# Optimization experiments

Measured on AMD Instinct MI355X. Metric: run time of the kernel, lower is better.

The kernel has to match this reference:

```python
import jax, jax.numpy as jnp
import numpy as np

E, K, CAP = 6, 2, 192
ALPHA, LOAD_PEN, MIN_USE, TEMP = 0.7, 2.0, 0.05, 1.0
BN_EPS = 1e-5
NEG = -1e30


def conv3x3(x, w, b=None):
    y = jax.lax.conv_general_dilated(x, w, (1, 1), 'SAME',
                                     dimension_numbers=('NCHW', 'OIHW', 'NCHW'))
    if b is not None:
        y = y + b[None, :, None, None]
    return y


def bn_eval(x, g, b):
    # fresh BatchNorm buffers: running_mean=0, running_var=1
    s = g / jnp.sqrt(1.0 + BN_EPS)
    return x * s[None, :, None, None] + b[None, :, None, None]


def maxpool2(x):
    return jax.lax.reduce_window(x, -jnp.inf, jax.lax.max,
                                 (1, 1, 2, 2), (1, 1, 2, 2), 'VALID')


def avgpool_to2(x):
    B, C, H, W = x.shape
    return x.reshape(B, C, 2, H // 2, 2, W // 2).mean(axis=(3, 5))


def expert_forward(p, x):
    h = jax.nn.relu(bn_eval(conv3x3(x, p['c1w'], p['c1b']), p['b1g'], p['b1b']))
    h = maxpool2(h)  # 32 -> 16
    h = jax.nn.relu(bn_eval(conv3x3(h, p['c2w'], p['c2b']), p['b2g'], p['b2b']))
    h = jax.nn.relu(bn_eval(conv3x3(h, p['c3w'], p['c3b']), p['b3g'], p['b3b']))
    h = maxpool2(h)  # 16 -> 8
    h = jax.nn.relu(bn_eval(conv3x3(h, p['c4w'], p['c4b']), p['b4g'], p['b4b']))
    h = jax.nn.relu(bn_eval(conv3x3(h, p['c5w'], p['c5b']), p['b5g'], p['b5b']))
    feat = h.mean(axis=(2, 3))                       # global avg pool -> [B, c3]
    f = jax.nn.relu(feat @ p['fw'].T + p['fb'])      # [B, feat_dim]
    return f @ p['cw'].T + p['cb']                   # [B, num_classes]


def moe_forward(x, t_c1w, t_b1g, t_b1b, t_c2w, t_b2g, t_b2b, t_fcw, t_fcb,
                g1w, g1b, g2w, g2b,
                e_c1w, e_c1b, e_b1g, e_b1b, e_c2w, e_c2b, e_b2g, e_b2b,
                e_c3w, e_c3b, e_b3g, e_b3b, e_c4w, e_c4b, e_b4g, e_b4b,
                e_c5w, e_c5b, e_b5g, e_b5b, e_fw, e_fb, e_cw, e_cb, ema):
    B = x.shape[0]
    # --- routing trunk ---
    h = jax.nn.relu(bn_eval(conv3x3(x, t_c1w), t_b1g, t_b1b))
    h = jax.nn.relu(bn_eval(conv3x3(h, t_c2w), t_b2g, t_b2b))
    h = avgpool_to2(maxpool2(h)).reshape(B, -1)      # [B, 128]
    rf = jax.nn.relu(h @ t_fcw.T + t_fcb)            # [B, routing_dim]
    # --- gate (eval: no dropout, no noise) ---
    g = jax.nn.relu(rf @ g1w.T + g1b)
    gate_scores = (g @ g2w.T + g2b) / TEMP           # [B, E]
    # --- all experts on full batch (dense, as in source) ---
    ep = {'c1w': e_c1w, 'c1b': e_c1b, 'b1g': e_b1g, 'b1b': e_b1b,
          'c2w': e_c2w, 'c2b': e_c2b, 'b2g': e_b2g, 'b2b': e_b2b,
          'c3w': e_c3w, 'c3b': e_c3b, 'b3g': e_b3g, 'b3b': e_b3b,
          'c4w': e_c4w, 'c4b': e_c4b, 'b4g': e_b4g, 'b4b': e_b4b,
          'c5w': e_c5w, 'c5b': e_c5b, 'b5g': e_b5g, 'b5b': e_b5b,
          'fw': e_fw, 'fb': e_fb, 'cw': e_cw, 'cb': e_cb}
    logits_e = jax.vmap(expert_forward, in_axes=(0, None))(ep, x)  # [E, B, C]
    logits_e = jnp.transpose(logits_e, (1, 0, 2))                   # [B, E, C]
    # confidence = -entropy = sum p*log(p)
    logp = jax.nn.log_softmax(logits_e, axis=2)
    conf = (jnp.exp(logp) * jnp.log(jnp.exp(logp) + 1e-12)).sum(axis=2)  # [B, E]
    # --- balanced scores ---
    combined = ALPHA * gate_scores + (1.0 - ALPHA) * conf
    boost = jnp.where(ema < MIN_USE, (MIN_USE - ema) * 10.0, 0.0)
    combined = combined + boost[None, :]
    balanced = combined - LOAD_PEN * ema[None, :]
    # --- greedy capacity-constrained dispatch (deterministic order, eval) ---
    _, topk_idx = jax.lax.top_k(balanced, K)          # [B, K]

    def step(loads, idxs):
        l = loads[idxs]                                # [K]
        fits = l < CAP
        first = jnp.argmax(fits)                       # first expert with room
        fallback = idxs[jnp.argmin(l)]
        chosen = jnp.where(fits.any(), idxs[first], fallback)
        return loads.at[chosen].add(1.0), chosen

    _, chosen = jax.lax.scan(step, jnp.zeros((E,), balanced.dtype), topk_idx)
    D = jax.nn.one_hot(chosen, E, dtype=bool)          # [B, E]
    # --- weighted combine ---
    masked = jnp.where(D, balanced, NEG)
    w = jax.nn.softmax(masked, axis=1) * D.astype(balanced.dtype)
    w = w / (w.sum(axis=1, keepdims=True) + 1e-12)
    logits_final = (w[:, :, None] * logits_e).sum(axis=1)  # [B, C]
    return logits_final, balanced, D


def _params(key):
    ks = iter(jax.random.split(key, 64))
    rd, rd2, fd, nc, c1, c2, c3 = 64, 32, 128, 10, 32, 64, 128

    def w(shape, fan):
        return jax.random.normal(next(ks), shape, jnp.float32) * np.sqrt(2.0 / fan)

    p = {}
    p['t_c1w'] = w((32, 3, 3, 3), 32 * 9); p['t_b1g'] = jnp.ones(32); p['t_b1b'] = jnp.zeros(32)
    p['t_c2w'] = w((32, 32, 3, 3), 32 * 9); p['t_b2g'] = jnp.ones(32); p['t_b2b'] = jnp.zeros(32)
    p['t_fcw'] = w((rd, 128), rd); p['t_fcb'] = jnp.zeros(rd)
    p['g1w'] = w((rd2, rd), rd2); p['g1b'] = jnp.zeros(rd2)
    p['g2w'] = w((E, rd2), E); p['g2b'] = jnp.zeros(E)
    for i, (ci, co) in enumerate([(3, c1), (c1, c2), (c2, c2), (c2, c3), (c3, c3)], 1):
        p[f'e_c{i}w'] = w((E, co, ci, 3, 3), co * 9)
        p[f'e_c{i}b'] = jnp.zeros((E, co))
        p[f'e_b{i}g'] = jnp.ones((E, co))
        p[f'e_b{i}b'] = jnp.zeros((E, co))
    p['e_fw'] = w((E, fd, c3), fd); p['e_fb'] = jnp.zeros((E, fd))
    p['e_cw'] = w((E, nc, fd), nc); p['e_cb'] = jnp.zeros((E, nc))
    p['ema'] = jnp.ones((E,), jnp.float32) / E
    return p


def setup_inputs() -> dict:
    key = jax.random.key(0)
    kx, kp = jax.random.split(key)
    inp = {'x': jax.random.normal(kx, (1024, 3, 32, 32), jnp.float32)}
    inp.update(_params(kp))
    return inp


def reference(x, t_c1w, t_b1g, t_b1b, t_c2w, t_b2g, t_b2b, t_fcw, t_fcb,
              g1w, g1b, g2w, g2b,
              e_c1w, e_c1b, e_b1g, e_b1b, e_c2w, e_c2b, e_b2g, e_b2b,
              e_c3w, e_c3b, e_b3g, e_b3b, e_c4w, e_c4b, e_b4g, e_b4b,
              e_c5w, e_c5b, e_b5g, e_b5b, e_fw, e_fb, e_cw, e_cb, ema):
    return moe_forward(x, t_c1w, t_b1g, t_b1b, t_c2w, t_b2g, t_b2b, t_fcw, t_fcb,
                       g1w, g1b, g2w, g2b,
                       e_c1w, e_c1b, e_b1g, e_b1b, e_c2w, e_c2b, e_b2g, e_b2b,
                       e_c3w, e_c3b, e_b3g, e_b3b, e_c4w, e_c4b, e_b4g, e_b4b,
                       e_c5w, e_c5b, e_b5g, e_b5b, e_fw, e_fb, e_cw, e_cb, ema)
```

## Files before the change

### kernel.cpp

```cpp
#include <hip/hip_runtime.h>
#include <math.h>

#define B_ 1024
#define E_ 6

typedef _Float16 half8 __attribute__((ext_vector_type(8)));
typedef float f32x4 __attribute__((ext_vector_type(4)));

__device__ __forceinline__ unsigned short h_bits(_Float16 h) {
    union { _Float16 f; unsigned short u; } c; c.f = h; return c.u;
}
__device__ __forceinline__ unsigned int splitpack(float v) {
    _Float16 h = (_Float16)v;
    _Float16 l = (_Float16)((v - (float)h) * 2048.0f);
    return (unsigned int)h_bits(h) | ((unsigned int)h_bits(l) << 16);
}
__device__ __forceinline__ int bswz(int fi, int p) { return fi ^ (((p >> 1) & 3) << 3); }

__global__ void prep_w(const float* __restrict__ w, const float* __restrict__ g,
                       float* __restrict__ wout, int CO, int CI, int total) {
    int i = blockIdx.x * 256 + threadIdx.x;
    if (i >= total) return;
    int k = i % 9;
    int t = i / 9;
    int ci = t % CI; t /= CI;
    int co = t % CO;
    int e  = t / CO;
    float s = g[e * CO + co] * (1.0f / sqrtf(1.0f + 1e-5f));
    wout[(((long)(e * CI + ci) * 9 + k) * CO) + co] = w[i] * s;
}

__global__ void prep_b(const float* __restrict__ cb, const float* __restrict__ g,
                       const float* __restrict__ bb, float* __restrict__ bout, int N) {
    int i = blockIdx.x * 256 + threadIdx.x;
    if (i >= N) return;
    float s = g[i] * (1.0f / sqrtf(1.0f + 1e-5f));
    float c = (cb != nullptr) ? cb[i] : 0.0f;
    bout[i] = c * s + bb[i];
}

__global__ void prep_wfrag(const float* __restrict__ w, const float* __restrict__ g,
                           _Float16* __restrict__ out, int CI, int CO, int total) {
    int i = blockIdx.x * 256 + threadIdx.x;
    if (i >= total) return;
    const int NC = CI / 32;
    const int NB = CO / 16;
    int j = i & 7;
    int lane = (i >> 3) & 63;
    int rest = i >> 9;
    int chunk = rest % NC; rest /= NC;
    int tap = rest % 9; rest /= 9;
    int nbg = rest % NB;
    int e = rest / NB;
    int co = nbg * 16 + (lane & 15);
    int ci = chunk * 32 + ((lane >> 4) * 8) + j;
    float s = g[e * CO + co] * (1.0f / sqrtf(1.0f + 1e-5f));
    float v = w[(((long)(e * CO + co) * CI + ci) * 9) + tap] * s;
    _Float16 hi = (_Float16)v;
    _Float16 lo = (_Float16)((v - (float)hi) * 2048.0f);
    long perE = (long)NB * 9 * NC * 2 * 512;
    long F0 = ((long)(nbg * 9 + tap) * NC + chunk) * 2;
    long base = (long)e * perE + F0 * 512 + lane * 8 + j;
    out[base] = hi;
    out[base + 512] = lo;
}

template <int CI, int CO, int H, int TS, int CO_BLK, int CI_CHUNK, bool POOL, int OUTMODE>
__launch_bounds__(256)
__global__ void conv3x3(const float* __restrict__ in, const float* __restrict__ wt,
                        const float* __restrict__ bias, void* __restrict__ outv) {
// ... 209 lines not shown
            for (int nb = 0; nb < 2; ++nb)
#pragma unroll
                for (int mb = 0; mb < 4; ++mb)
                    accL[mb * 2 + nb] = __builtin_amdgcn_mfma_f32_16x16x32_f16(
                        ah[mb], bl[nb], accL[mb * 2 + nb], 0, 0, 0);
#pragma unroll
            for (int nb = 0; nb < 2; ++nb)
#pragma unroll
                for (int mb = 0; mb < 4; ++mb)
                    accL[mb * 2 + nb] = __builtin_amdgcn_mfma_f32_16x16x32_f16(
                        al[mb], bh[nb], accL[mb * 2 + nb], 0, 0, 0);
        }

    const float inv2048 = 1.0f / 2048.0f;
    float bv[2];
#pragma unroll
    for (int nb = 0; nb < 2; ++nb) bv[nb] = bias[nb * 16 + l15];
    float avg[2] = {0.0f, 0.0f};
#pragma unroll
    for (int k = 0; k < 2; ++k)
#pragma unroll
        for (int j = 0; j < 2; ++j)
#pragma unroll
            for (int nb = 0; nb < 2; ++nb) {
                float m = -1e30f;
#pragma unroll
                for (int dm = 0; dm < 2; ++dm)
#pragma unroll
                    for (int dr = 0; dr < 2; ++dr) {
                        int a = (2 * k + dm) * 2 + nb;
                        int r = 2 * j + dr;
                        float v = accH[a][r] + accL[a][r] * inv2048 + bv[nb];
                        m = fmaxf(m, v);
                    }
                avg[nb] += fmaxf(m, 0.0f);
            }
#pragma unroll
    for (int nb = 0; nb < 2; ++nb) {
        avg[nb] += __shfl_xor(avg[nb], 16);
        avg[nb] += __shfl_xor(avg[nb], 32);
    }
    if (q == 0) {
        red[wv][l15] = avg[0];
        red[wv][16 + l15] = avg[1];
    }
    __syncthreads();
    if (tid < 32) {
        float s = red[0][tid] + red[1][tid] + red[2][tid] + red[3][tid];
        int n = n0 + nl;
        rf[(long)n * 128 + tid * 4 + (tile >> 1) * 2 + (tile & 1)] = s * (1.0f / 64.0f);
    }
}

__launch_bounds__(256, 2)
__global__ void conv_c12(const float* __restrict__ x,
                         const float* __restrict__ w1, const float* __restrict__ b1,
                         const _Float16* __restrict__ wt2, const float* __restrict__ b2,
                         unsigned int* __restrict__ outp) {
    __shared__ float xs[3 * 1156];
    __shared__ float w1s[864];
    __shared__ float b1s[32];
    __shared__ _Float16 ldsH[18 * 18 * 40];
    __shared__ _Float16 ldsL[18 * 18 * 40];

    const int tid = threadIdx.x;
    const int wv = tid >> 6, lane = tid & 63;
    const int q = lane >> 4, l15 = lane & 15;
    const int n = blockIdx.x;

    {
        half8 z = {};
        half8* zh = (half8*)ldsH;
        half8* zl = (half8*)ldsL;
        for (int i = tid; i < 18 * 18 * 40 / 8; i += 256) { zh[i] = z; zl[i] = z; }
    }
    for (int i = tid; i < 864; i += 256) w1s[i] = w1[i];
    if (tid < 32) b1s[tid] = b1[tid];
    for (int i = tid; i < 3 * 1156; i += 256) {
        int c = i / 1156;
        int r = i - c * 1156;
        int yy = r / 34 - 1, xx = r % 34 - 1;
        float v = 0.0f;
        if ((unsigned)yy < 32u && (unsigned)xx < 32u)
            v = x[((long)n * 3 + c) * 1024 + yy * 32 + xx];
        xs[i] = v;
    }
    __syncthreads();

    {
        const int py = tid >> 4, px = tid & 15;
#pragma unroll
        for (int cog = 0; cog < 4; ++cog) {
            float a[4][8];
#pragma unroll
            for (int j = 0; j < 8; ++j) {
                float bv = b1s[cog * 8 + j];
#pragma unroll
                for (int p = 0; p < 4; ++p) a[p][j] = bv;
            }
            for (int ci = 0; ci < 3; ++ci) {
                float patch[16];
#pragma unroll
                for (int r = 0; r < 4; ++r)
#pragma unroll
                    for (int cpx = 0; cpx < 4; ++cpx)
                        patch[r * 4 + cpx] = xs[ci * 1156 + (2 * py + r) * 34 + (2 * px + cpx)];
#pragma unroll
                for (int ky = 0; ky < 3; ++ky)
#pragma unroll
                    for (int kx = 0; kx < 3; ++kx) {
                        const float* wr = &w1s[((ci * 3 + ky) * 3 + kx) * 32 + cog * 8];
#pragma unroll
                        for (int j = 0; j < 8; ++j) {
                            float wvv = wr[j];
#pragma unroll
                            for (int dy = 0; dy < 2; ++dy)
#pragma unroll
                                for (int dx = 0; dx < 2; ++dx)
                                    a[dy * 2 + dx][j] =
                                        fmaf(patch[(dy + ky) * 4 + (dx + kx)], wvv,
                                             a[dy * 2 + dx][j]);
                        }
                    }
            }
            int fibase = ((py + 1) * 18 + (px + 1)) * 40 + cog * 8;
#pragma unroll
            for (int j = 0; j < 8; ++j) {
                float m = fmaxf(fmaxf(a[0][j], a[1][j]), fmaxf(a[2][j], a[3][j]));
                m = fmaxf(m, 0.0f);
                _Float16 hi = (_Float16)m;
                _Float16 lo = (_Float16)((m - (float)hi) * 2048.0f);
                ldsH[fibase + j] = hi;
                ldsL[fibase + j] = lo;
            }
        }
    }
    __syncthreads();

    f32x4 accH[16], accL[16];
#pragma unroll
    for (int i = 0; i < 16; ++i) { accH[i] = (f32x4){0,0,0,0}; accL[i] = (f32x4){0,0,0,0}; }

#pragma unroll
    for (int ky = 0; ky < 3; ++ky)
#pragma unroll
        for (int kx = 0; kx < 3; ++kx) {
            const int tap = ky * 3 + kx;
            half8 ah[4], al[4];
#pragma unroll
            for (int mb = 0; mb < 4; ++mb) {
                int y = wv * 4 + mb;
                int fi = ((y + ky) * 18 + (l15 + kx)) * 40 + q * 8;
                ah[mb] = *(const half8*)&ldsH[fi];
                al[mb] = *(const half8*)&ldsL[fi];
            }
            half8 bh[4], bl[4];
#pragma unroll
            for (int nb = 0; nb < 4; ++nb) {
                int F0 = (nb * 9 + tap) * 2;
                bh[nb] = ((const half8*)wt2)[(long)F0 * 64 + lane];
                bl[nb] = ((const half8*)wt2)[(long)(F0 + 1) * 64 + lane];
            }
#pragma unroll
            for (int nb = 0; nb < 4; ++nb)
#pragma unroll
                for (int mb = 0; mb < 4; ++mb)
                    accH[mb * 4 + nb] = __builtin_amdgcn_mfma_f32_16x16x32_f16(
                        ah[mb], bh[nb], accH[mb * 4 + nb], 0, 0, 0);
#pragma unroll
            for (int nb = 0; nb < 4; ++nb)
#pragma unroll
                for (int mb = 0; mb < 4; ++mb)
                    accL[mb * 4 + nb] = __builtin_amdgcn_mfma_f32_16x16x32_f16(
                        ah[mb], bl[nb], accL[mb * 4 + nb], 0, 0, 0);
#pragma unroll
            for (int nb = 0; nb < 4; ++nb)
#pragma unroll
                for (int mb = 0; mb < 4; ++mb)
                    accL[mb * 4 + nb] = __builtin_amdgcn_mfma_f32_16x16x32_f16(
                        al[mb], bh[nb], accL[mb * 4 + nb], 0, 0, 0);
        }

    const float inv2048 = 1.0f / 2048.0f;
    float bv[4];
#pragma unroll
    for (int nb = 0; nb < 4; ++nb) bv[nb] = b2[nb * 16 + l15];
#pragma unroll
    for (int mb = 0; mb < 4; ++mb) {
        int y = wv * 4 + mb;
#pragma unroll
        for (int r = 0; r < 4; ++r) {
            int px = y * 16 + q * 4 + r;
            long base = ((long)n * 256 + px) * 64;
#pragma unroll
            for (int nb = 0; nb < 4; ++nb) {
                float v = accH[mb * 4 + nb][r] + accL[mb * 4 + nb][r] * inv2048 + bv[nb];
                v = fmaxf(v, 0.0f);
                outp[base + nb * 16 + l15] = splitpack(v);
            }
        }
    }
}

__launch_bounds__(256, 2)
__global__ void conv_c345(const unsigned int* __restrict__ in,
                          const _Float16* __restrict__ wt3, const float* __restrict__ b3,
                          const _Float16* __restrict__ wt4, const float* __restrict__ b4,
                          const _Float16* __restrict__ wt5, const float* __restrict__ b5,
                          float* __restrict__ feat) {
    __shared__ _Float16 poolA[25920];
    __shared__ _Float16 poolB[12800];
    _Float16* AH = poolA;
    _Float16* AL = poolA + 12960;
    _Float16* CH = poolA;
    _Float16* CL = poolA + 12800;
    _Float16* BH = poolB;
    _Float16* BL = poolB + 6400;

    const int tid = threadIdx.x;
    const int wv = tid >> 6, lane = tid & 63;
    const int q = lane >> 4, l15 = lane & 15;
    const int n = blockIdx.x;
    const float inv2048 = 1.0f / 2048.0f;

    {
        half8 z = {};
        half8* za = (half8*)poolA;
        for (int i = tid; i < 3240; i += 256) za[i] = z;
        half8* zb = (half8*)poolB;
        for (int i = tid; i < 1600; i += 256) zb[i] = z;
    }

    f32x4 accH[16], accL[16];
#pragma unroll
    for (int i = 0; i < 16; ++i) { accH[i] = (f32x4){0,0,0,0}; accL[i] = (f32x4){0,0,0,0}; }

    for (int c = 0; c < 2; ++c) {
        __syncthreads();
        for (int v = tid; v < 2048; v += 256) {
            int cu = v & 7;
            int px = v >> 3;
            long gidx = ((long)n * 256 + px) * 64 + c * 32 + cu * 4;
            uint4 w = *(const uint4*)(in + gidx);
            unsigned int h01 = (w.x & 0xffffu) | (w.y << 16);
            unsigned int h23 = (w.z & 0xffffu) | (w.w << 16);
            unsigned int l01 = (w.x >> 16) | (w.y & 0xffff0000u);
            unsigned int l23 = (w.z >> 16) | (w.w & 0xffff0000u);
            int py = px >> 4, pxx = px & 15;
            int fi = ((py + 1) * 18 + (pxx + 1)) * 40 + cu * 4;
            *(uint2*)(&AH[fi]) = make_uint2(h01, h23);
            *(uint2*)(&AL[fi]) = make_uint2(l01, l23);
        }
        __syncthreads();

#pragma unroll
        for (int ky = 0; ky < 3; ++ky)
#pragma unroll
            for (int kx = 0; kx < 3; ++kx) {
                const int tap = ky * 3 + kx;
                half8 ah[4], al[4];
#pragma unroll
                for (int mb = 0; mb < 4; ++mb) {
                    int y = wv * 4 + mb;
                    int fi = ((y + ky) * 18 + (l15 + kx)) * 40 + q * 8;
                    ah[mb] = *(const half8*)&AH[fi];
                    al[mb] = *(const half8*)&AL[fi];
                }
                half8 bh[4], bl[4];
#pragma unroll
                for (int nb = 0; nb < 4; ++nb) {
                    int F0 = ((nb * 9 + tap) * 2 + c) * 2;
                    bh[nb] = ((const half8*)wt3)[(long)F0 * 64 + lane];
                    bl[nb] = ((const half8*)wt3)[(long)(F0 + 1) * 64 + lane];
                }
#pragma unroll
                for (int nb = 0; nb < 4; ++nb)
#pragma unroll
                    for (int mb = 0; mb < 4; ++mb)
                        accH[mb * 4 + nb] = __builtin_amdgcn_mfma_f32_16x16x32_f16(
                            ah[mb], bh[nb], accH[mb * 4 + nb], 0, 0, 0);
#pragma unroll
                for (int nb = 0; nb < 4; ++nb)
#pragma unroll
                    for (int mb = 0; mb < 4; ++mb)
                        accL[mb * 4 + nb] = __builtin_amdgcn_mfma_f32_16x16x32_f16(
                            ah[mb], bl[nb], accL[mb * 4 + nb], 0, 0, 0);
#pragma unroll
                for (int nb = 0; nb < 4; ++nb)
#pragma unroll
                    for (int mb = 0; mb < 4; ++mb)
                        accL[mb * 4 + nb] = __builtin_amdgcn_mfma_f32_16x16x32_f16(
                            al[mb], bh[nb], accL[mb * 4 + nb], 0, 0, 0);
            }
    }
    __syncthreads();

    {
        half8 z = {};
        half8* za = (half8*)poolA;
        for (int i = tid; i < 3240; i += 256) za[i] = z;
    }
    {
        float bv[4];
#pragma unroll
        for (int nb = 0; nb < 4; ++nb) bv[nb] = b3[nb * 16 + l15];
#pragma unroll
        for (int k = 0; k < 2; ++k)
#pragma unroll
            for (int j = 0; j < 2; ++j) {
                int yy = wv * 2 + k;
                int xx = q * 2 + j;
                int p = (yy + 1) * 10 + (xx + 1);
#pragma unroll
                for (int nb = 0; nb < 4; ++nb) {
                    float m = -1e30f;
#pragma unroll
                    for (int dm = 0; dm < 2; ++dm)
#pragma unroll
                        for (int dr = 0; dr < 2; ++dr) {
                            int a = (2 * k + dm) * 4 + nb;
                            int r = 2 * j + dr;
                            float v = accH[a][r] + accL[a][r] * inv2048 + bv[nb];
                            m = fmaxf(m, v);
                        }
                    m = fmaxf(m, 0.0f);
                    _Float16 hi = (_Float16)m;
                    _Float16 lo = (_Float16)((m - (float)hi) * 2048.0f);
                    int ci = nb * 16 + l15;
                    int bi = bswz((ci >> 5) * 3200 + p * 32 + (ci & 31), p);
                    BH[bi] = hi;
                    BL[bi] = lo;
                }
            }
    }
    __syncthreads();

#pragma unroll
    for (int i = 0; i < 8; ++i) { accH[i] = (f32x4){0,0,0,0}; accL[i] = (f32x4){0,0,0,0}; }

    for (int c = 0; c < 2; ++c) {
#pragma unroll
        for (int ky = 0; ky < 3; ++ky)
#pragma unroll
            for (int kx = 0; kx < 3; ++kx) {
                const int tap = ky * 3 + kx;
                half8 ah[4], al[4];
#pragma unroll
                for (int mb = 0; mb < 4; ++mb) {
                    int m = mb * 16 + l15;
                    int p = ((m >> 3) + ky) * 10 + ((m & 7) + kx);
                    int fi = bswz(c * 3200 + p * 32 + q * 8, p);
                    ah[mb] = *(const half8*)&BH[fi];
                    al[mb] = *(const half8*)&BL[fi];
                }
                half8 bh[2], bl[2];
#pragma unroll
                for (int nb = 0; nb < 2; ++nb) {
                    int nbg = wv * 2 + nb;
                    int F0 = ((nbg * 9 + tap) * 2 + c) * 2;
                    bh[nb] = ((const half8*)wt4)[(long)F0 * 64 + lane];
                    bl[nb] = ((const half8*)wt4)[(long)(F0 + 1) * 64 + lane];
                }
#pragma unroll
                for (int nb = 0; nb < 2; ++nb)
#pragma unroll
                    for (int mb = 0; mb < 4; ++mb)
                        accH[mb * 2 + nb] = __builtin_amdgcn_mfma_f32_16x16x32_f16(
                            ah[mb], bh[nb], accH[mb * 2 + nb], 0, 0, 0);
#pragma unroll
                for (int nb = 0; nb < 2; ++nb)
#pragma unroll
                    for (int mb = 0; mb < 4; ++mb)
                        accL[mb * 2 + nb] = __builtin_amdgcn_mfma_f32_16x16x32_f16(
                            ah[mb], bl[nb], accL[mb * 2 + nb], 0, 0, 0);
#pragma unroll
                for (int nb = 0; nb < 2; ++nb)
#pragma unroll
                    for (int mb = 0; mb < 4; ++mb)
                        accL[mb * 2 + nb] = __builtin_amdgcn_mfma_f32_16x16x32_f16(
                            al[mb], bh[nb], accL[mb * 2 + nb], 0, 0, 0);
            }
    }

    {
        float bv[2];
#pragma unroll
        for (int nb = 0; nb < 2; ++nb) bv[nb] = b4[wv * 32 + nb * 16 + l15];
#pragma unroll
        for (int mb = 0; mb < 4; ++mb)
#pragma unroll
            for (int r = 0; r < 4; ++r) {
                int px = mb * 16 + q * 4 + r;
                int p = ((px >> 3) + 1) * 10 + ((px & 7) + 1);
#pragma unroll
                for (int nb = 0; nb < 2; ++nb) {
                    float v = accH[mb * 2 + nb][r] + accL[mb * 2 + nb][r] * inv2048 + bv[nb];
                    v = fmaxf(v, 0.0f);
                    _Float16 hi = (_Float16)v;
                    _Float16 lo = (_Float16)((v - (float)hi) * 2048.0f);
                    int ci = nb * 16 + l15;
                    int fi = bswz(wv * 3200 + p * 32 + ci, p);
                    CH[fi] = hi;
                    CL[fi] = lo;
                }
            }
    }
    __syncthreads();

#pragma unroll
    for (int i = 0; i < 8; ++i) { accH[i] = (f32x4){0,0,0,0}; accL[i] = (f32x4){0,0,0,0}; }

    for (int c = 0; c < 4; ++c) {
#pragma unroll
        for (int ky = 0; ky < 3; ++ky)
#pragma unroll
            for (int kx = 0; kx < 3; ++kx) {
                const int tap = ky * 3 + kx;
                half8 ah[4], al[4];
#pragma unroll
                for (int mb = 0; mb < 4; ++mb) {
                    int m = mb * 16 + l15;
                    int p = ((m >> 3) + ky) * 10 + ((m & 7) + kx);
                    int fi = bswz(c * 3200 + p * 32 + q * 8, p);
                    ah[mb] = *(const half8*)&CH[fi];
                    al[mb] = *(const half8*)&CL[fi];
                }
                half8 bh[2], bl[2];
#pragma unroll
                for (int nb = 0; nb < 2; ++nb) {
                    int nbg = wv * 2 + nb;
                    int F0 = ((nbg * 9 + tap) * 4 + c) * 2;
                    bh[nb] = ((const half8*)wt5)[(long)F0 * 64 + lane];
                    bl[nb] = ((const half8*)wt5)[(long)(F0 + 1) * 64 + lane];
                }
#pragma unroll
                for (int nb = 0; nb < 2; ++nb)
#pragma unroll
                    for (int mb = 0; mb < 4; ++mb)
                        accH[mb * 2 + nb] = __builtin_amdgcn_mfma_f32_16x16x32_f16(
                            ah[mb], bh[nb], accH[mb * 2 + nb], 0, 0, 0);
#pragma unroll
                for (int nb = 0; nb < 2; ++nb)
#pragma unroll
                    for (int mb = 0; mb < 4; ++mb)
                        accL[mb * 2 + nb] = __builtin_amdgcn_mfma_f32_16x16x32_f16(
                            ah[mb], bl[nb], accL[mb * 2 + nb], 0, 0, 0);
#pragma unroll
                for (int nb = 0; nb < 2; ++nb)
#pragma unroll
                    for (int mb = 0; mb < 4; ++mb)
                        accL[mb * 2 + nb] = __builtin_amdgcn_mfma_f32_16x16x32_f16(
                            al[mb], bh[nb], accL[mb * 2 + nb], 0, 0, 0);
            }
    }

    {
        float bv[2];
#pragma unroll
        for (int nb = 0; nb < 2; ++nb) bv[nb] = b5[wv * 32 + nb * 16 + l15];
        float s0 = 0.0f, s1 = 0.0f;
#pragma unroll
        for (int mb = 0; mb < 4; ++mb)
#pragma unroll
            for (int r = 0; r < 4; ++r) {
                float v0 = accH[mb * 2 + 0][r] + accL[mb * 2 + 0][r] * inv2048 + bv[0];
                float v1 = accH[mb * 2 + 1][r] + accL[mb * 2 + 1][r] * inv2048 + bv[1];
                s0 += fmaxf(v0, 0.0f);
                s1 += fmaxf(v1, 0.0f);
            }
        s0 += __shfl_xor(s0, 16); s0 += __shfl_xor(s0, 32);
        s1 += __shfl_xor(s1, 16); s1 += __shfl_xor(s1, 32);
        if (lane < 16) {
            long fb_ = (long)n * 128 + wv * 32 + l15;
            feat[fb_] = s0 * (1.0f / 64.0f);
            feat[fb_ + 16] = s1 * (1.0f / 64.0f);
        }
    }
}

__launch_bounds__(128)
__global__ void head_k(const float* __restrict__ feat, const float* __restrict__ fw,
                       const float* __restrict__ fb, const float* __restrict__ cw,
                       const float* __restrict__ cb, float* __restrict__ outl) {
    __shared__ float fe[128];
    __shared__ float fv[128];
    int n = blockIdx.x, t = threadIdx.x;
    fe[t] = feat[(long)n * 128 + t];
    __syncthreads();
    const float* wr = fw + t * 128;
    float a = fb[t];
#pragma unroll 8
    for (int k = 0; k < 128; ++k) a = fmaf(fe[k], wr[k], a);
    fv[t] = fmaxf(a, 0.0f);
    __syncthreads();
    if (t < 10) {
        const float* cr = cw + t * 128;
        float a2 = cb[t];
#pragma unroll 8
        for (int k = 0; k < 128; ++k) a2 = fmaf(fv[k], cr[k], a2);
        outl[n * 10 + t] = a2;
    }
}

template <int I, int O, bool RELU>
__global__ void fc_k(const float* __restrict__ in, const float* __restrict__ W,
                     const float* __restrict__ bias, float* __restrict__ out) {
    int g = blockIdx.x * 256 + threadIdx.x;
    if (g >= B_ * O) return;
    int n = g / O;
    int o = g - n * O;
    const float* ip = in + (long)n * I;
    const float* wp = W + (long)o * I;
    float a = bias[o];
#pragma unroll 8
    for (int k = 0; k < I; ++k) a = fmaf(ip[k], wp[k], a);
    if (RELU) a = fmaxf(a, 0.0f);
    out[g] = a;
}

__global__ void conf_bal_k(const float* __restrict__ logitsE, const float* __restrict__ gate,
                           const float* __restrict__ ema, float* __restrict__ balanced,
                           unsigned char* __restrict__ cand) {
    int b = blockIdx.x * 256 + threadIdx.x;
    if (b >= B_) return;
    float bal[E_];
#pragma unroll
    for (int e = 0; e < E_; ++e) {
        const float* lp = logitsE + ((long)e * B_ + b) * 10;
        float m = lp[0];
// ... 113 lines not shown
    float* rf_in   = ws + o; o += B_ * 128;
    float* rf      = ws + o; o += B_ * 64;
    float* gv      = ws + o; o += B_ * 32;
    float* gate    = ws + o; o += B_ * E_;
    float* logitsE = ws + o; o += E_ * B_ * 10;
    float* featb   = ws + o; o += B_ * 128;
    int*   chosen  = (int*)(ws + o); o += B_;
    unsigned char* cand = (unsigned char*)(ws + o); o += 256;
    float* wt_t1 = ws + o; o += 864;
    float* bt_t1 = ws + o; o += 32;
    float* bt_t2 = ws + o; o += 32;
    float* wt_c1 = ws + o; o += 6 * 864;
    float* bt_c1 = ws + o; o += 6 * 32;
    float* bt_c2 = ws + o; o += 6 * 64;
    float* bt_c3 = ws + o; o += 6 * 64;
    float* bt_c4 = ws + o; o += 6 * 128;
    float* bt_c5 = ws + o; o += 6 * 128;
    _Float16* wfrag_t2 = (_Float16*)(ws + o); o += 9216;
    _Float16* wfrag_c2 = (_Float16*)(ws + o); o += 110592;
    _Float16* wfrag_c3 = (_Float16*)(ws + o); o += 221184;
    _Float16* wfrag_c4 = (_Float16*)(ws + o); o += 442368;
    _Float16* wfrag_c5 = (_Float16*)(ws + o); o += 884736;

    unsigned int* R2u = (unsigned int*)R2f;
    (void)R1f;

    auto gsz = [](int n) { return (n + 255) / 256; };
    prep_w<<<gsz(864), 256, 0, stream>>>(t_c1w, t_b1g, wt_t1, 32, 3, 864);
    prep_b<<<1, 256, 0, stream>>>(nullptr, t_b1g, t_b1b, bt_t1, 32);
    prep_wfrag<<<gsz(9216), 256, 0, stream>>>(t_c2w, t_b2g, wfrag_t2, 32, 32, 9216);
    prep_b<<<1, 256, 0, stream>>>(nullptr, t_b2g, t_b2b, bt_t2, 32);
    prep_w<<<gsz(5184), 256, 0, stream>>>(e_c1w, e_b1g, wt_c1, 32, 3, 5184);
    prep_b<<<1, 256, 0, stream>>>(e_c1b, e_b1g, e_b1b, bt_c1, 192);
    prep_wfrag<<<gsz(110592), 256, 0, stream>>>(e_c2w, e_b2g, wfrag_c2, 32, 64, 110592);
    prep_b<<<2, 256, 0, stream>>>(e_c2b, e_b2g, e_b2b, bt_c2, 384);
    prep_wfrag<<<gsz(221184), 256, 0, stream>>>(e_c3w, e_b3g, wfrag_c3, 64, 64, 221184);
    prep_b<<<2, 256, 0, stream>>>(e_c3b, e_b3g, e_b3b, bt_c3, 384);
    prep_wfrag<<<gsz(442368), 256, 0, stream>>>(e_c4w, e_b4g, wfrag_c4, 64, 128, 442368);
    prep_b<<<3, 256, 0, stream>>>(e_c4b, e_b4g, e_b4b, bt_c4, 768);
    prep_wfrag<<<gsz(884736), 256, 0, stream>>>(e_c5w, e_b5g, wfrag_c5, 128, 128, 884736);
    prep_b<<<3, 256, 0, stream>>>(e_c5b, e_b5g, e_b5b, bt_c5, 768);

    for (int q = 0; q < 2; ++q) {
        const float* xq = x + (size_t)q * 512 * 3 * 1024;
        conv3x3<3, 32, 32, 16, 32, 3, false, 1><<<512 * 4, 256, 0, stream>>>(
            xq, wt_t1, bt_t1, (void*)R2u);
        conv_mfma_t2<<<512 * 4, 256, 0, stream>>>(R2u, wfrag_t2, bt_t2, rf_in, q * 512);
    }
    fc_k<128, 64, true><<<256, 256, 0, stream>>>(rf_in, t_fcw, t_fcb, rf);
    fc_k<64, 32, true><<<128, 256, 0, stream>>>(rf, g1w, g1b, gv);
    fc_k<32, 6, false><<<24, 256, 0, stream>>>(gv, g2w, g2b, gate);

    for (int e = 0; e < E_; ++e) {
        conv_c12<<<B_, 256, 0, stream>>>(
            x, wt_c1 + e * 864, bt_c1 + e * 32,
            wfrag_c2 + (size_t)e * 36864, bt_c2 + e * 64, R2u);
        conv_c345<<<B_, 256, 0, stream>>>(
            R2u, wfrag_c3 + (size_t)e * 73728, bt_c3 + e * 64,
            wfrag_c4 + (size_t)e * 147456, bt_c4 + e * 128,
            wfrag_c5 + (size_t)e * 294912, bt_c5 + e * 128, featb);
        head_k<<<B_, 128, 0, stream>>>(featb, e_fw + e * 16384, e_fb + e * 128,
                                       e_cw + e * 1280, e_cb + e * 10,
                                       logitsE + (size_t)e * B_ * 10);
    }

    float* balanced = out + B_ * 10;
    conf_bal_k<<<4, 256, 0, stream>>>(logitsE, gate, ema, balanced, cand);
    dispatch_k<<<1, 64, 0, stream>>>(cand, chosen);
    final_k<<<4, 256, 0, stream>>>(logitsE, chosen, out);
}
```

Before: 1.596 ms.

## Fuse expert conv1-2 and conv3-5 kernels into one 512-thread kernel

Merges conv_c12 and conv_c345 into one conv_expert kernel per image. The conv2 output now stays in shared memory as split-fp16 instead of making a round trip through global memory via R2u. The block grows to 512 threads (8 waves), and work is split so each wave covers half the output channels or a single 16-channel slice. Only the halo borders are zeroed, and the bank swizzle is dropped. The costs are higher LDS use (about 155KB per block), which limits occupancy, and possible bank conflicts without the swizzle.

```diff
diff --git a/kernel.cpp b/kernel.cpp
--- a/kernel.cpp
+++ b/kernel.cpp
@@ -15,7 +15,6 @@
     _Float16 l = (_Float16)((v - (float)h) * 2048.0f);
     return (unsigned int)h_bits(h) | ((unsigned int)h_bits(l) << 16);
 }
-__device__ __forceinline__ int bswz(int fi, int p) { return fi ^ (((p >> 1) & 3) << 3); }
 
 __global__ void prep_w(const float* __restrict__ w, const float* __restrict__ g,
                        float* __restrict__ wout, int CO, int CI, int total) {
@@ -331,31 +330,42 @@
     }
 }
 
-__launch_bounds__(256, 2)
-__global__ void conv_c12(const float* __restrict__ x,
-                         const float* __restrict__ w1, const float* __restrict__ b1,
-                         const _Float16* __restrict__ wt2, const float* __restrict__ b2,
-                         unsigned int* __restrict__ outp) {
-    __shared__ float xs[3 * 1156];
-    __shared__ float w1s[864];
-    __shared__ float b1s[32];
-    __shared__ _Float16 ldsH[18 * 18 * 40];
-    __shared__ _Float16 ldsL[18 * 18 * 40];
+__launch_bounds__(512, 2)
+__global__ void conv_expert(const float* __restrict__ x,
+                            const float* __restrict__ w1, const float* __restrict__ b1,
+                            const _Float16* __restrict__ wt2, const float* __restrict__ b2,
+                            const _Float16* __restrict__ wt3, const float* __restrict__ b3,
+                            const _Float16* __restrict__ wt4, const float* __restrict__ b4,
+                            const _Float16* __restrict__ wt5, const float* __restrict__ b5,
+                            float* __restrict__ feat) {
+    __shared__ _Float16 pool[77760];
+    _Float16* c2H = pool;
+    _Float16* c2L = pool + 12960;
+    _Float16* BH  = pool;
+    _Float16* BL  = pool + 6400;
+    float* xs  = (float*)(pool + 25920);
+    float* w1s = (float*)(pool + 25920 + 6936);
+    float* b1s = (float*)(pool + 25920 + 6936 + 1728);
+    _Float16* AH = pool + 25920;
+    _Float16* AL = pool + 51840;
+    _Float16* CH = pool + 25920;
+    _Float16* CL = pool + 38720;
 
     const int tid = threadIdx.x;
     const int wv = tid >> 6, lane = tid & 63;
     const int q = lane >> 4, l15 = lane & 15;
+    const int rg = wv >> 1, ch2 = wv & 1;
     const int n = blockIdx.x;
+    const float inv2048 = 1.0f / 2048.0f;
 
     {
         half8 z = {};
-        half8* zh = (half8*)ldsH;
-        half8* zl = (half8*)ldsL;
-        for (int i = tid; i < 18 * 18 * 40 / 8; i += 256) { zh[i] = z; zl[i] = z; }
-    }
-    for (int i = tid; i < 864; i += 256) w1s[i] = w1[i];
+        half8* zp = (half8*)pool;
+        for (int i = tid; i < 3240; i += 512) zp[i] = z;
+    }
+    for (int i = tid; i < 864; i += 512) w1s[i] = w1[i];
     if (tid < 32) b1s[tid] = b1[tid];
-    for (int i = tid; i < 3 * 1156; i += 256) {
+    for (int i = tid; i < 3 * 1156; i += 512) {
         int c = i / 1156;
         int r = i - c * 1156;
         int yy = r / 34 - 1, xx = r % 34 - 1;
@@ -367,15 +377,18 @@
     __syncthreads();
 
     {
-        const int py = tid >> 4, px = tid & 15;
-#pragma unroll
-        for (int cog = 0; cog < 4; ++cog) {
+        const int pix = tid & 255;
+        const int py1 = pix >> 4, px1 = pix & 15;
+        const int coh = tid >> 8;
+#pragma unroll
+        for (int cg = 0; cg < 2; ++cg) {
+            const int cog = coh * 2 + cg;
             float a[4][8];
 #pragma unroll
             for (int j = 0; j < 8; ++j) {
-                float bv = b1s[cog * 8 + j];
-#pragma unroll
-                for (int p = 0; p < 4; ++p) a[p][j] = bv;
+                float bvv = b1s[cog * 8 + j];
+#pragma unroll
+                for (int p = 0; p < 4; ++p) a[p][j] = bvv;
             }
             for (int ci = 0; ci < 3; ++ci) {
                 float patch[16];
@@ -383,7 +396,7 @@
                 for (int r = 0; r < 4; ++r)
 #pragma unroll
                     for (int cpx = 0; cpx < 4; ++cpx)
-                        patch[r * 4 + cpx] = xs[ci * 1156 + (2 * py + r) * 34 + (2 * px + cpx)];
+                        patch[r * 4 + cpx] = xs[ci * 1156 + (2 * py1 + r) * 34 + (2 * px1 + cpx)];
 #pragma unroll
                 for (int ky = 0; ky < 3; ++ky)
 #pragma unroll
@@ -402,23 +415,38 @@
                         }
                     }
             }
-            int fibase = ((py + 1) * 18 + (px + 1)) * 40 + cog * 8;
+            int fibase = ((py1 + 1) * 18 + (px1 + 1)) * 40 + cog * 8;
 #pragma unroll
             for (int j = 0; j < 8; ++j) {
                 float m = fmaxf(fmaxf(a[0][j], a[1][j]), fmaxf(a[2][j], a[3][j]));
                 m = fmaxf(m, 0.0f);
                 _Float16 hi = (_Float16)m;
                 _Float16 lo = (_Float16)((m - (float)hi) * 2048.0f);
-                ldsH[fibase + j] = hi;
-                ldsL[fibase + j] = lo;
+                c2H[fibase + j] = hi;
+                c2L[fibase + j] = lo;
             }
         }
     }
     __syncthreads();
 
-    f32x4 accH[16], accL[16];
-#pragma unroll
-    for (int i = 0; i < 16; ++i) { accH[i] = (f32x4){0,0,0,0}; accL[i] = (f32x4){0,0,0,0}; }
+    for (int u = tid; u < 2 * 68 * 5; u += 512) {
+        int g = u % 5;
+        int t2 = u / 5;
+        int ck = t2 / 68;
+        int rp = t2 % 68;
+        int wy, wx;
+        if (rp < 18) { wy = 0; wx = rp; }
+        else if (rp < 36) { wy = 17; wx = rp - 18; }
+        else if (rp < 52) { wy = rp - 35; wx = 0; }
+        else { wy = rp - 51; wx = 17; }
+        int fi = ck * 12960 + (wy * 18 + wx) * 40 + g * 8;
+        *(uint4*)(&AH[fi]) = make_uint4(0, 0, 0, 0);
+        *(uint4*)(&AL[fi]) = make_uint4(0, 0, 0, 0);
+    }
+
+    f32x4 accH[8], accL[8];
+#pragma unroll
+    for (int i = 0; i < 8; ++i) { accH[i] = (f32x4){0,0,0,0}; accL[i] = (f32x4){0,0,0,0}; }
 
 #pragma unroll
     for (int ky = 0; ky < 3; ++ky)
@@ -428,110 +456,67 @@
             half8 ah[4], al[4];
 #pragma unroll
             for (int mb = 0; mb < 4; ++mb) {
-                int y = wv * 4 + mb;
+                int y = rg * 4 + mb;
                 int fi = ((y + ky) * 18 + (l15 + kx)) * 40 + q * 8;
-                ah[mb] = *(const half8*)&ldsH[fi];
-                al[mb] = *(const half8*)&ldsL[fi];
-            }
-            half8 bh[4], bl[4];
-#pragma unroll
-            for (int nb = 0; nb < 4; ++nb) {
-                int F0 = (nb * 9 + tap) * 2;
+                ah[mb] = *(const half8*)&c2H[fi];
+                al[mb] = *(const half8*)&c2L[fi];
+            }
+            half8 bh[2], bl[2];
+#pragma unroll
+            for (int nb = 0; nb < 2; ++nb) {
+                int nbg = ch2 * 2 + nb;
+                int F0 = (nbg * 9 + tap) * 2;
                 bh[nb] = ((const half8*)wt2)[(long)F0 * 64 + lane];
                 bl[nb] = ((const half8*)wt2)[(long)(F0 + 1) * 64 + lane];
             }
 #pragma unroll
-            for (int nb = 0; nb < 4; ++nb)
-#pragma unroll
-                for (int mb = 0; mb < 4; ++mb)
-                    accH[mb * 4 + nb] = __builtin_amdgcn_mfma_f32_16x16x32_f16(
-                        ah[mb], bh[nb], accH[mb * 4 + nb], 0, 0, 0);
-#pragma unroll
-            for (int nb = 0; nb < 4; ++nb)
-#pragma unroll
-                for (int mb = 0; mb < 4; ++mb)
-                    accL[mb * 4 + nb] = __builtin_amdgcn_mfma_f32_16x16x32_f16(
-                        ah[mb], bl[nb], accL[mb * 4 + nb], 0, 0, 0);
-#pragma unroll
-            for (int nb = 0; nb < 4; ++nb)
-#pragma unroll
-                for (int mb = 0; mb < 4; ++mb)
-                    accL[mb * 4 + nb] = __builtin_amdgcn_mfma_f32_16x16x32_f16(
-                        al[mb], bh[nb], accL[mb * 4 + nb], 0, 0, 0);
-        }
-
-    const float inv2048 = 1.0f / 2048.0f;
-    float bv[4];
-#pragma unroll
-    for (int nb = 0; nb < 4; ++nb) bv[nb] = b2[nb * 16 + l15];
-#pragma unroll
-    for (int mb = 0; mb < 4; ++mb) {
-        int y = wv * 4 + mb;
-#pragma unroll
-        for (int r = 0; r < 4; ++r) {
-            int px = y * 16 + q * 4 + r;
-            long base = ((long)n * 256 + px) * 64;
-#pragma unroll
-            for (int nb = 0; nb < 4; ++nb) {
-                float v = accH[mb * 4 + nb][r] + accL[mb * 4 + nb][r] * inv2048 + bv[nb];
-                v = fmaxf(v, 0.0f);
-                outp[base + nb * 16 + l15] = splitpack(v);
-            }
-        }
-    }
-}
-
-__launch_bounds__(256, 2)
-__global__ void conv_c345(const unsigned int* __restrict__ in,
-                          const _Float16* __restrict__ wt3, const float* __restrict__ b3,
-                          const _Float16* __restrict__ wt4, const float* __restrict__ b4,
-                          const _Float16* __restrict__ wt5, const float* __restrict__ b5,
-                          float* __restrict__ feat) {
-    __shared__ _Float16 poolA[25920];
-    __shared__ _Float16 poolB[12800];
-    _Float16* AH = poolA;
-    _Float16* AL = poolA + 12960;
-    _Float16* CH = poolA;
-    _Float16* CL = poolA + 12800;
-    _Float16* BH = poolB;
-    _Float16* BL = poolB + 6400;
-
-    const int tid = threadIdx.x;
-    const int wv = tid >> 6, lane = tid & 63;
-    const int q = lane >> 4, l15 = lane & 15;
-    const int n = blockIdx.x;
-    const float inv2048 = 1.0f / 2048.0f;
-
+            for (int nb = 0; nb < 2; ++nb)
+#pragma unroll
+                for (int mb = 0; mb < 4; ++mb)
+                    accH[mb * 2 + nb] = __builtin_amdgcn_mfma_f32_16x16x32_f16(
+                        ah[mb], bh[nb], accH[mb * 2 + nb], 0, 0, 0);
+#pragma unroll
+            for (int nb = 0; nb < 2; ++nb)
+#pragma unroll
+                for (int mb = 0; mb < 4; ++mb)
+                    accL[mb * 2 + nb] = __builtin_amdgcn_mfma_f32_16x16x32_f16(
+                        ah[mb], bl[nb], accL[mb * 2 + nb], 0, 0, 0);
+#pragma unroll
+            for (int nb = 0; nb < 2; ++nb)
+#pragma unroll
+                for (int mb = 0; mb < 4; ++mb)
+                    accL[mb * 2 + nb] = __builtin_amdgcn_mfma_f32_16x16x32_f16(
+                        al[mb], bh[nb], accL[mb * 2 + nb], 0, 0, 0);
+        }
     {
-        half8 z = {};
-        half8* za = (half8*)poolA;
-        for (int i = tid; i < 3240; i += 256) za[i] = z;
-        half8* zb = (half8*)poolB;
-        for (int i = tid; i < 1600; i += 256) zb[i] = z;
-    }
-
-    f32x4 accH[16], accL[16];
-#pragma unroll
-    for (int i = 0; i < 16; ++i) { accH[i] = (f32x4){0,0,0,0}; accL[i] = (f32x4){0,0,0,0}; }
+        float bv[2];
+#pragma unroll
+        for (int nb = 0; nb < 2; ++nb) bv[nb] = b2[ch2 * 32 + nb * 16 + l15];
+#pragma unroll
+        for (int mb = 0; mb < 4; ++mb) {
+            int y = rg * 4 + mb;
+#pragma unroll
+            for (int r = 0; r < 4; ++r) {
+                int p = (y + 1) * 18 + (q * 4 + r + 1);
+#pragma unroll
+                for (int nb = 0; nb < 2; ++nb) {
+                    float v = accH[mb * 2 + nb][r] + accL[mb * 2 + nb][r] * inv2048 + bv[nb];
+                    v = fmaxf(v, 0.0f);
+                    _Float16 hi = (_Float16)v;
+                    _Float16 lo = (_Float16)((v - (float)hi) * 2048.0f);
+                    int fi = ch2 * 12960 + p * 40 + nb * 16 + l15;
+                    AH[fi] = hi;
+                    AL[fi] = lo;
+                }
+            }
+        }
+    }
+    __syncthreads();
+
+#pragma unroll
+    for (int i = 0; i < 8; ++i) { accH[i] = (f32x4){0,0,0,0}; accL[i] = (f32x4){0,0,0,0}; }
 
     for (int c = 0; c < 2; ++c) {
-        __syncthreads();
-        for (int v = tid; v < 2048; v += 256) {
-            int cu = v & 7;
-            int px = v >> 3;
-            long gidx = ((long)n * 256 + px) * 64 + c * 32 + cu * 4;
-            uint4 w = *(const uint4*)(in + gidx);
-            unsigned int h01 = (w.x & 0xffffu) | (w.y << 16);
-            unsigned int h23 = (w.z & 0xffffu) | (w.w << 16);
-            unsigned int l01 = (w.x >> 16) | (w.y & 0xffff0000u);
-            unsigned int l23 = (w.z >> 16) | (w.w & 0xffff0000u);
-            int py = px >> 4, pxx = px & 15;
-            int fi = ((py + 1) * 18 + (pxx + 1)) * 40 + cu * 4;
-            *(uint2*)(&AH[fi]) = make_uint2(h01, h23);
-            *(uint2*)(&AL[fi]) = make_uint2(l01, l23);
-        }
-        __syncthreads();
-
 #pragma unroll
         for (int ky = 0; ky < 3; ++ky)
 #pragma unroll
@@ -540,64 +525,88 @@
                 half8 ah[4], al[4];
 #pragma unroll
                 for (int mb = 0; mb < 4; ++mb) {
-                    int y = wv * 4 + mb;
-                    int fi = ((y + ky) * 18 + (l15 + kx)) * 40 + q * 8;
+                    int y = rg * 4 + mb;
+                    int fi = c * 12960 + ((y + ky) * 18 + (l15 + kx)) * 40 + q * 8;
                     ah[mb] = *(const half8*)&AH[fi];
                     al[mb] = *(const half8*)&AL[fi];
                 }
-                half8 bh[4], bl[4];
-#pragma unroll
-                for (int nb = 0; nb < 4; ++nb) {
-                    int F0 = ((nb * 9 + tap) * 2 + c) * 2;
+                half8 bh[2], bl[2];
+#pragma unroll
+                for (int nb = 0; nb < 2; ++nb) {
+                    int nbg = ch2 * 2 + nb;
+                    int F0 = ((nbg * 9 + tap) * 2 + c) * 2;
                     bh[nb] = ((const half8*)wt3)[(long)F0 * 64 + lane];
                     bl[nb] = ((const half8*)wt3)[(long)(F0 + 1) * 64 + lane];
                 }
 #pragma unroll
-                for (int nb = 0; nb < 4; ++nb)
+                for (int nb = 0; nb < 2; ++nb)
 #pragma unroll
                     for (int mb = 0; mb < 4; ++mb)
-                        accH[mb * 4 + nb] = __builtin_amdgcn_mfma_f32_16x16x32_f16(
-                            ah[mb], bh[nb], accH[mb * 4 + nb], 0, 0, 0);
-#pragma unroll
-                for (int nb = 0; nb < 4; ++nb)
+                        accH[mb * 2 + nb] = __builtin_amdgcn_mfma_f32_16x16x32_f16(
+                            ah[mb], bh[nb], accH[mb * 2 + nb], 0, 0, 0);
+#pragma unroll
+                for (int nb = 0; nb < 2; ++nb)
 #pragma unroll
                     for (int mb = 0; mb < 4; ++mb)
-                        accL[mb * 4 + nb] = __builtin_amdgcn_mfma_f32_16x16x32_f16(
-                            ah[mb], bl[nb], accL[mb * 4 + nb], 0, 0, 0);
-#pragma unroll
-                for (int nb = 0; nb < 4; ++nb)
+                        accL[mb * 2 + nb] = __builtin_amdgcn_mfma_f32_16x16x32_f16(
+                            ah[mb], bl[nb], accL[mb * 2 + nb], 0, 0, 0);
+#pragma unroll
+                for (int nb = 0; nb < 2; ++nb)
 #pragma unroll
                     for (int mb = 0; mb < 4; ++mb)
-                        accL[mb * 4 + nb] = __builtin_amdgcn_mfma_f32_16x16x32_f16(
-                            al[mb], bh[nb], accL[mb * 4 + nb], 0, 0, 0);
+                        accL[mb * 2 + nb] = __builtin_amdgcn_mfma_f32_16x16x32_f16(
+                            al[mb], bh[nb], accL[mb * 2 + nb], 0, 0, 0);
             }
     }
     __syncthreads();
 
+    for (int u = tid; u < 2 * 36 * 4; u += 512) {
+        int g = u & 3;
+        int t2 = u >> 2;
+        int ck = t2 / 36;
+        int rp = t2 % 36;
+        int wy, wx;
+        if (rp < 10) { wy = 0; wx = rp; }
+        else if (rp < 20) { wy = 9; wx = rp - 10; }
+        else if (rp < 28) { wy = rp - 19; wx = 0; }
+        else { wy = rp - 27; wx = 9; }
+        int fi = ck * 3200 + (wy * 10 + wx) * 32 + g * 8;
+        *(uint4*)(&BH[fi]) = make_uint4(0, 0, 0, 0);
+        *(uint4*)(&BL[fi]) = make_uint4(0, 0, 0, 0);
+    }
+    for (int u = tid; u < 4 * 36 * 4; u += 512) {
+        int g = u & 3;
+        int t2 = u >> 2;
+        int ck = t2 / 36;
+        int rp = t2 % 36;
+        int wy, wx;
+        if (rp < 10) { wy = 0; wx = rp; }
+        else if (rp < 20) { wy = 9; wx = rp - 10; }
+        else if (rp < 28) { wy = rp - 19; wx = 0; }
+        else { wy = rp - 27; wx = 9; }
+        int fi = ck * 3200 + (wy * 10 + wx) * 32 + g * 8;
+        *(uint4*)(&CH[fi]) = make_uint4(0, 0, 0, 0);
+        *(uint4*)(&CL[fi]) = make_uint4(0, 0, 0, 0);
+    }
     {
-        half8 z = {};
-        half8* za = (half8*)poolA;
-        for (int i = tid; i < 3240; i += 256) za[i] = z;
-    }
-    {
-        float bv[4];
-#pragma unroll
-        for (int nb = 0; nb < 4; ++nb) bv[nb] = b3[nb * 16 + l15];
+        float bv[2];
+#pragma unroll
+        for (int nb = 0; nb < 2; ++nb) bv[nb] = b3[ch2 * 32 + nb * 16 + l15];
 #pragma unroll
         for (int k = 0; k < 2; ++k)
 #pragma unroll
             for (int j = 0; j < 2; ++j) {
-                int yy = wv * 2 + k;
+                int yy = rg * 2 + k;
                 int xx = q * 2 + j;
                 int p = (yy + 1) * 10 + (xx + 1);
 #pragma unroll
-                for (int nb = 0; nb < 4; ++nb) {
+                for (int nb = 0; nb < 2; ++nb) {
                     float m = -1e30f;
 #pragma unroll
                     for (int dm = 0; dm < 2; ++dm)
 #pragma unroll
                         for (int dr = 0; dr < 2; ++dr) {
-                            int a = (2 * k + dm) * 4 + nb;
+                            int a = (2 * k + dm) * 2 + nb;
                             int r = 2 * j + dr;
                             float v = accH[a][r] + accL[a][r] * inv2048 + bv[nb];
                             m = fmaxf(m, v);
@@ -605,17 +614,16 @@
                     m = fmaxf(m, 0.0f);
                     _Float16 hi = (_Float16)m;
                     _Float16 lo = (_Float16)((m - (float)hi) * 2048.0f);
-                    int ci = nb * 16 + l15;
-                    int bi = bswz((ci >> 5) * 3200 + p * 32 + (ci & 31), p);
-                    BH[bi] = hi;
-                    BL[bi] = lo;
+                    int fi = ch2 * 3200 + p * 32 + nb * 16 + l15;
+                    BH[fi] = hi;
+                    BL[fi] = lo;
                 }
             }
     }
     __syncthreads();
 
 #pragma unroll
-    for (int i = 0; i < 8; ++i) { accH[i] = (f32x4){0,0,0,0}; accL[i] = (f32x4){0,0,0,0}; }
+    for (int i = 0; i < 4; ++i) { accH[i] = (f32x4){0,0,0,0}; accL[i] = (f32x4){0,0,0,0}; }
 
     for (int c = 0; c < 2; ++c) {
 #pragma unroll
@@ -628,66 +636,48 @@
                 for (int mb = 0; mb < 4; ++mb) {
                     int m = mb * 16 + l15;
                     int p = ((m >> 3) + ky) * 10 + ((m & 7) + kx);
-                    int fi = bswz(c * 3200 + p * 32 + q * 8, p);
+                    int fi = c * 3200 + p * 32 + q * 8;
                     ah[mb] = *(const half8*)&BH[fi];
                     al[mb] = *(const half8*)&BL[fi];
                 }
-                half8 bh[2], bl[2];
-#pragma unroll
-                for (int nb = 0; nb < 2; ++nb) {
-                    int nbg = wv * 2 + nb;
-                    int F0 = ((nbg * 9 + tap) * 2 + c) * 2;
-                    bh[nb] = ((const half8*)wt4)[(long)F0 * 64 + lane];
-                    bl[nb] = ((const half8*)wt4)[(long)(F0 + 1) * 64 + lane];
-                }
-#pragma unroll
-                for (int nb = 0; nb < 2; ++nb)
-#pragma unroll
-                    for (int mb = 0; mb < 4; ++mb)
-                        accH[mb * 2 + nb] = __builtin_amdgcn_mfma_f32_16x16x32_f16(
-                            ah[mb], bh[nb], accH[mb * 2 + nb], 0, 0, 0);
-#pragma unroll
-                for (int nb = 0; nb < 2; ++nb)
-#pragma unroll
-                    for (int mb = 0; mb < 4; ++mb)
-                        accL[mb * 2 + nb] = __builtin_amdgcn_mfma_f32_16x16x32_f16(
-                            ah[mb], bl[nb], accL[mb * 2 + nb], 0, 0, 0);
-#pragma unroll
-                for (int nb = 0; nb < 2; ++nb)
-#pragma unroll
-                    for (int mb = 0; mb < 4; ++mb)
-                        accL[mb * 2 + nb] = __builtin_amdgcn_mfma_f32_16x16x32_f16(
-                            al[mb], bh[nb], accL[mb * 2 + nb], 0, 0, 0);
-            }
-    }
-
+                half8 bh, bl;
+                {
+                    int F0 = ((wv * 9 + tap) * 2 + c) * 2;
+                    bh = ((const half8*)wt4)[(long)F0 * 64 + lane];
+                    bl = ((const half8*)wt4)[(long)(F0 + 1) * 64 + lane];
+                }
+#pragma unroll
+                for (int mb = 0; mb < 4; ++mb)
+                    accH[mb] = __builtin_amdgcn_mfma_f32_16x16x32_f16(ah[mb], bh, accH[mb], 0, 0, 0);
+#pragma unroll
+                for (int mb = 0; mb < 4; ++mb)
+                    accL[mb] = __builtin_amdgcn_mfma_f32_16x16x32_f16(ah[mb], bl, accL[mb], 0, 0, 0);
+#pragma unroll
+                for (int mb = 0; mb < 4; ++mb)
+                    accL[mb] = __builtin_amdgcn_mfma_f32_16x16x32_f16(al[mb], bh, accL[mb], 0, 0, 0);
+            }
+    }
     {
-        float bv[2];
-#pragma unroll
-        for (int nb = 0; nb < 2; ++nb) bv[nb] = b4[wv * 32 + nb * 16 + l15];
+        float bv = b4[wv * 16 + l15];
 #pragma unroll
         for (int mb = 0; mb < 4; ++mb)
 #pragma unroll
             for (int r = 0; r < 4; ++r) {
                 int px = mb * 16 + q * 4 + r;
                 int p = ((px >> 3) + 1) * 10 + ((px & 7) + 1);
-#pragma unroll
-                for (int nb = 0; nb < 2; ++nb) {
-                    float v = accH[mb * 2 + nb][r] + accL[mb * 2 + nb][r] * inv2048 + bv[nb];
-                    v = fmaxf(v, 0.0f);
-                    _Float16 hi = (_Float16)v;
-                    _Float16 lo = (_Float16)((v - (float)hi) * 2048.0f);
-                    int ci = nb * 16 + l15;
-                    int fi = bswz(wv * 3200 + p * 32 + ci, p);
-                    CH[fi] = hi;
-                    CL[fi] = lo;
-                }
+                float v = accH[mb][r] + accL[mb][r] * inv2048 + bv;
+                v = fmaxf(v, 0.0f);
+                _Float16 hi = (_Float16)v;
+                _Float16 lo = (_Float16)((v - (float)hi) * 2048.0f);
+                int fi = (wv >> 1) * 3200 + p * 32 + (wv & 1) * 16 + l15;
+                CH[fi] = hi;
+                CL[fi] = lo;
             }
     }
     __syncthreads();
 
 #pragma unroll
-    for (int i = 0; i < 8; ++i) { accH[i] = (f32x4){0,0,0,0}; accL[i] = (f32x4){0,0,0,0}; }
+    for (int i = 0; i < 4; ++i) { accH[i] = (f32x4){0,0,0,0}; accL[i] = (f32x4){0,0,0,0}; }
 
     for (int c = 0; c < 4; ++c) {
 #pragma unroll
@@ -700,60 +690,41 @@
                 for (int mb = 0; mb < 4; ++mb) {
                     int m = mb * 16 + l15;
                     int p = ((m >> 3) + ky) * 10 + ((m & 7) + kx);
-                    int fi = bswz(c * 3200 + p * 32 + q * 8, p);
+                    int fi = c * 3200 + p * 32 + q * 8;
                     ah[mb] = *(const half8*)&CH[fi];
                     al[mb] = *(const half8*)&CL[fi];
                 }
-                half8 bh[2], bl[2];
-#pragma unroll
-                for (int nb = 0; nb < 2; ++nb) {
-                    int nbg = wv * 2 + nb;
-                    int F0 = ((nbg * 9 + tap) * 4 + c) * 2;
-                    bh[nb] = ((const half8*)wt5)[(long)F0 * 64 + lane];
-                    bl[nb] = ((const half8*)wt5)[(long)(F0 + 1) * 64 + lane];
-                }
-#pragma unroll
-                for (int nb = 0; nb < 2; ++nb)
-#pragma unroll
-                    for (int mb = 0; mb < 4; ++mb)
-                        accH[mb * 2 + nb] = __builtin_amdgcn_mfma_f32_16x16x32_f16(
-                            ah[mb], bh[nb], accH[mb * 2 + nb], 0, 0, 0);
-#pragma unroll
-                for (int nb = 0; nb < 2; ++nb)
-#pragma unroll
-                    for (int mb = 0; mb < 4; ++mb)
-                        accL[mb * 2 + nb] = __builtin_amdgcn_mfma_f32_16x16x32_f16(
-                            ah[mb], bl[nb], accL[mb * 2 + nb], 0, 0, 0);
-#pragma unroll
-                for (int nb = 0; nb < 2; ++nb)
-#pragma unroll
-                    for (int mb = 0; mb < 4; ++mb)
-                        accL[mb * 2 + nb] = __builtin_amdgcn_mfma_f32_16x16x32_f16(
-                            al[mb], bh[nb], accL[mb * 2 + nb], 0, 0, 0);
-            }
-    }
-
+                half8 bh, bl;
+                {
+                    int F0 = ((wv * 9 + tap) * 4 + c) * 2;
+                    bh = ((const half8*)wt5)[(long)F0 * 64 + lane];
+                    bl = ((const half8*)wt5)[(long)(F0 + 1) * 64 + lane];
+                }
+#pragma unroll
+                for (int mb = 0; mb < 4; ++mb)
+                    accH[mb] = __builtin_amdgcn_mfma_f32_16x16x32_f16(ah[mb], bh, accH[mb], 0, 0, 0);
+#pragma unroll
+                for (int mb = 0; mb < 4; ++mb)
+                    accL[mb] = __builtin_amdgcn_mfma_f32_16x16x32_f16(ah[mb], bl, accL[mb], 0, 0, 0);
+#pragma unroll
+                for (int mb = 0; mb < 4; ++mb)
+                    accL[mb] = __builtin_amdgcn_mfma_f32_16x16x32_f16(al[mb], bh, accL[mb], 0, 0, 0);
+            }
+    }
     {
-        float bv[2];
-#pragma unroll
-        for (int nb = 0; nb < 2; ++nb) bv[nb] = b5[wv * 32 + nb * 16 + l15];
-        float s0 = 0.0f, s1 = 0.0f;
+        float bv = b5[wv * 16 + l15];
+        float s = 0.0f;
 #pragma unroll
         for (int mb = 0; mb < 4; ++mb)
 #pragma unroll
             for (int r = 0; r < 4; ++r) {
-                float v0 = accH[mb * 2 + 0][r] + accL[mb * 2 + 0][r] * inv2048 + bv[0];
-                float v1 = accH[mb * 2 + 1][r] + accL[mb * 2 + 1][r] * inv2048 + bv[1];
-                s0 += fmaxf(v0, 0.0f);
-                s1 += fmaxf(v1, 0.0f);
-            }
-        s0 += __shfl_xor(s0, 16); s0 += __shfl_xor(s0, 32);
-        s1 += __shfl_xor(s1, 16); s1 += __shfl_xor(s1, 32);
-        if (lane < 16) {
-            long fb_ = (long)n * 128 + wv * 32 + l15;
-            feat[fb_] = s0 * (1.0f / 64.0f);
-            feat[fb_ + 16] = s1 * (1.0f / 64.0f);
-        }
+                float v = accH[mb][r] + accL[mb][r] * inv2048 + bv;
+                s += fmaxf(v, 0.0f);
+            }
+        s += __shfl_xor(s, 16);
+        s += __shfl_xor(s, 32);
+        if (lane < 16)
+            feat[(long)n * 128 + wv * 16 + l15] = s * (1.0f / 64.0f);
     }
 }
 
@@ -973,11 +944,10 @@
     fc_k<32, 6, false><<<24, 256, 0, stream>>>(gv, g2w, g2b, gate);
 
     for (int e = 0; e < E_; ++e) {
-        conv_c12<<<B_, 256, 0, stream>>>(
+        conv_expert<<<B_, 512, 0, stream>>>(
             x, wt_c1 + e * 864, bt_c1 + e * 32,
-            wfrag_c2 + (size_t)e * 36864, bt_c2 + e * 64, R2u);
-        conv_c345<<<B_, 256, 0, stream>>>(
-            R2u, wfrag_c3 + (size_t)e * 73728, bt_c3 + e * 64,
+            wfrag_c2 + (size_t)e * 36864, bt_c2 + e * 64,
+            wfrag_c3 + (size_t)e * 73728, bt_c3 + e * 64,
             wfrag_c4 + (size_t)e * 147456, bt_c4 + e * 128,
             wfrag_c5 + (size_t)e * 294912, bt_c5 + e * 128, featb);
         head_k<<<B_, 128, 0, stream>>>(featb, e_fw + e * 16384, e_fb + e * 128,
```

Measured after the change: 1.323 ms. 1.21x faster.
